# Performance work log

Hardware: AMD Instinct MI355X
Metric: run time of the kernel (lower is better)

Reference implementation:

```python
import jax, jax.numpy as jnp
import numpy as np

HEAD_SIZE = 64


def setup_inputs() -> dict:
    key = jax.random.key(0)
    ks = jax.random.split(key, 4)
    B, S, H, D = 8, 4096, 768, HEAD_SIZE
    scale = 1.0 / np.sqrt(H)
    return {
        "x": jax.random.normal(ks[0], (B, S, H), dtype=jnp.float32),
        "Wq": jax.random.normal(ks[1], (H, D), dtype=jnp.float32) * scale,
        "bq": jnp.zeros((D,), dtype=jnp.float32),
        "Wk": jax.random.normal(ks[2], (H, D), dtype=jnp.float32) * scale,
        "bk": jnp.zeros((D,), dtype=jnp.float32),
        "Wv": jax.random.normal(ks[3], (H, D), dtype=jnp.float32) * scale,
        "bv": jnp.zeros((D,), dtype=jnp.float32),
    }


def reference(x, Wq, bq, Wk, bk, Wv, bv):
    # x: [B, S, H]
    B, S, H = x.shape
    D = Wq.shape[1]
    q = x @ Wq + bq  # [B, S, D]
    k = x @ Wk + bk
    v = x @ Wv + bv
    # naive full score matrix [B, S, S]
    scores = jnp.einsum("bsd,btd->bst", q, k)
    causal = jnp.tril(jnp.ones((S, S), dtype=bool))  # lower-triangular mask
    scores = jnp.where(causal[None, :, :], scores, -jnp.inf)
    attn = jax.nn.softmax(scores / jnp.sqrt(jnp.float32(D)), axis=-1)
    # dropout is identity in eval/deterministic reference
    out = jnp.einsum("bst,btd->bsd", attn, v)  # [B, S, D]
    return out
```

## Files before the change

kernel.cpp:

```cpp
#include <hip/hip_runtime.h>

typedef unsigned short u16;
typedef __bf16 bf16_t;
typedef bf16_t bf16x8 __attribute__((ext_vector_type(8)));
typedef float f32x4 __attribute__((ext_vector_type(4)));
typedef u16 u16x8 __attribute__((ext_vector_type(8)));
typedef u16 u16x4 __attribute__((ext_vector_type(4)));
typedef unsigned u32x4 __attribute__((ext_vector_type(4)));

#define B_ 8
#define S_ 4096
#define H_ 768
#define M_ (B_ * S_)

__device__ __forceinline__ u16 f2b(float f) {
  unsigned u = __float_as_uint(f);
  u += 0x7fffu + ((u >> 16) & 1u);
  return (u16)(u >> 16);
}

__device__ __forceinline__ void gl_lds16(const void* g, void* l) {
  __builtin_amdgcn_global_load_lds(
      (const __attribute__((address_space(1))) void*)g,
      (__attribute__((address_space(3))) void*)l, 16, 0, 0);
}

__global__ __launch_bounds__(256) void wconv_k(const float* __restrict__ Wq,
                                               const float* __restrict__ Wk,
                                               const float* __restrict__ Wv,
                                               u16* __restrict__ WbT) {
  __shared__ float wt[64 * 68];
  const int tid = threadIdx.x;
  int mat = blockIdx.x / 12;
  int k0 = (blockIdx.x % 12) * 64;
  const float* W = (mat == 0) ? Wq : ((mat == 1) ? Wk : Wv);
  int r = tid >> 2, c0 = (tid & 3) * 16;
  const float* src = W + (size_t)(k0 + r) * 64 + c0;
#pragma unroll
  for (int j = 0; j < 16; j += 4)
    *(float4*)&wt[r * 68 + c0 + j] = *(const float4*)(src + j);
  __syncthreads();
  int d = tid >> 2;
  u16* dst = WbT + (size_t)(mat * 64 + d) * 768 + k0 + c0;
  u16x8 o0, o1;
#pragma unroll
  for (int j = 0; j < 8; ++j) o0[j] = f2b(wt[(c0 + j) * 68 + d]);
#pragma unroll
  for (int j = 0; j < 8; ++j) o1[j] = f2b(wt[(c0 + 8 + j) * 68 + d]);
  *(u16x8*)dst = o0;
  *(u16x8*)(dst + 8) = o1;
}

__global__ __launch_bounds__(256) void qkv_k(const float* __restrict__ x,
                                             const u16* __restrict__ WbT,
                                             const float* __restrict__ bq,
                                             const float* __restrict__ bk,
                                             const float* __restrict__ bv,
                                             u16* __restrict__ qb,
                                             u16* __restrict__ kb,
                                             u16* __restrict__ vbT) {
  __shared__ __align__(16) u16 smem[2 * 2560 + 2 * 7680];
  const int tid = threadIdx.x;
  const int w = tid >> 6, ln = tid & 15, qd = (tid >> 4) & 3;
  const int row0 = blockIdx.x * 64;

  const f32x4 z4 = {0.f, 0.f, 0.f, 0.f};
  f32x4 acc[4][3];
#pragma unroll
  for (int rt = 0; rt < 4; ++rt)
#pragma unroll
    for (int ct = 0; ct < 3; ++ct) acc[rt][ct] = z4;

  const int xr = tid >> 2, xc = (tid & 3) * 8;
  float4 xf0, xf1;
  u16x8 wf[3];

  auto load_t = [&](int kt) {
    const float* sx = x + (size_t)(row0 + xr) * 768 + kt * 32 + xc;
    xf0 = *(const float4*)sx;
    xf1 = *(const float4*)(sx + 4);
#pragma unroll
    for (int i = 0; i < 3; ++i) {
      int c = i * 256 + tid;
      int r = c >> 2, off = (c & 3) * 8;
      wf[i] = *(const u16x8*)(WbT + (size_t)r * 768 + kt * 32 + off);
    }
  };

  load_t(0);
  for (int kt = 0; kt < 24; ++kt) {
    u16* xs = smem + (kt & 1) * 2560;
    u16* wsb = smem + 5120 + (kt & 1) * 7680;
    {
      u16x8 v;
      v[0] = f2b(xf0.x); v[1] = f2b(xf0.y); v[2] = f2b(xf0.z); v[3] = f2b(xf0.w);
      v[4] = f2b(xf1.x); v[5] = f2b(xf1.y); v[6] = f2b(xf1.z); v[7] = f2b(xf1.w);
      *(u16x8*)&xs[xr * 40 + xc] = v;
#pragma unroll
      for (int i = 0; i < 3; ++i) {
        int c = i * 256 + tid;
        int r = c >> 2, off = (c & 3) * 8;
        *(u16x8*)&wsb[r * 40 + off] = wf[i];
      }
    }
    if (kt < 23) load_t(kt + 1);
    __syncthreads();
    bf16x8 af[4], bfr[3];
#pragma unroll
    for (int rt = 0; rt < 4; ++rt)
      af[rt] = *(const bf16x8*)&xs[(rt * 16 + ln) * 40 + qd * 8];
#pragma unroll
    for (int ct = 0; ct < 3; ++ct)
      bfr[ct] = *(const bf16x8*)&wsb[(w * 48 + ct * 16 + ln) * 40 + qd * 8];
#pragma unroll
    for (int rt = 0; rt < 4; ++rt)
#pragma unroll
      for (int ct = 0; ct < 3; ++ct)
        acc[rt][ct] = __builtin_amdgcn_mfma_f32_16x16x32_bf16(
            af[rt], bfr[ct], acc[rt][ct], 0, 0, 0);
    __syncthreads();
  }

  u16* vt = smem;
#pragma unroll
  for (int ct = 0; ct < 3; ++ct) {
    int col = w * 48 + ct * 16 + ln;
    int mat = col >> 6, d = col & 63;
    if (mat < 2) {
      const float* bp = (mat == 0) ? bq : bk;
      u16* op = (mat == 0) ? qb : kb;
      float bias = bp[d];
      float scale = (mat == 0) ? 0.18033688011112042f : 1.0f;
#pragma unroll
      for (int rt = 0; rt < 4; ++rt)
#pragma unroll
        for (int r = 0; r < 4; ++r)
          op[(size_t)(row0 + rt * 16 + qd * 4 + r) * 64 + d] =
              f2b((acc[rt][ct][r] + bias) * scale);
    } else {
      float bias = bv[d];
#pragma unroll
      for (int rt = 0; rt < 4; ++rt)
#pragma unroll
        for (int r = 0; r < 4; ++r)
          vt[d * 72 + rt * 16 + qd * 4 + r] = f2b(acc[rt][ct][r] + bias);
    }
  }
  __syncthreads();
  {
    int d = tid >> 2, so = (tid & 3) * 16;
    int b = row0 >> 12, s0 = row0 & 4095;
    u16* dst = vbT + ((size_t)b * 64 + d) * 4096 + s0;
#pragma unroll
    for (int g = 0; g < 4; ++g) {
      int ts = so + g * 4;
      int tn = (ts & 0x23) | ((ts & 4) << 2) | ((ts & 0x18) >> 1);
      *(u16x4*)(dst + ts) = *(const u16x4*)&vt[d * 72 + tn];
    }
  }
}

__global__ __launch_bounds__(256) void attn_k(const u16* __restrict__ qb,
                                              const u16* __restrict__ kb,
                                              const u16* __restrict__ vbT,
                                              float* __restrict__ po,
                                              float* __restrict__ pl) {
  __shared__ __align__(16) u16 ks[3][4096];
  __shared__ __align__(16) u16 vs[3][4096];
  const int tid = threadIdx.x;
  const int wv = tid >> 6, ln = tid & 15, qd = (tid >> 4) & 3;
  const int id = blockIdx.x;
  const int b = id & 7;
  const int j = id >> 3;
  int qi = 31, acc = 0;
  while (acc + ((qi >> 3) + 1) <= j) {
    acc += (qi >> 3) + 1;
    --qi;
  }
  const int c = j - acc;
  const int ntiles = 2 * qi + 2;
  const int nc = (qi >> 3) + 1;
  const int bas = ntiles / nc, rem = ntiles % nc;
  const int tstart = c * bas + (c < rem ? c : rem);
  const int tcount = bas + (c < rem ? 1 : 0);
  const int q0 = qi * 128;
  const int q0w = q0 + wv * 32;
  const int base = b * S_;
  const u16* kg = kb + (size_t)base * 64;
  const u16* vg = vbT + (size_t)b * 64 * 4096;

  bf16x8 qf[2][2];
#pragma unroll
  for (int qt = 0; qt < 2; ++qt) {
    const u16* qrow = qb + (size_t)(base + q0w + qt * 16 + ln) * 64;
    qf[qt][0] = *(const bf16x8*)(qrow + qd * 8);
    qf[qt][1] = *(const bf16x8*)(qrow + 32 + qd * 8);
  }
  const f32x4 z4 = {0.f, 0.f, 0.f, 0.f};
  f32x4 o0[4] = {z4, z4, z4, z4};
  f32x4 o1[4] = {z4, z4, z4, z4};
  float lq0 = 0.f, lq1 = 0.f;
  const int lr = (tid & 63) >> 3, csl = tid & 7;

  auto prefetch = [&](int bufi, int tile) {
    const u16* kt_ = kg + (size_t)tile * 4096;
    const u16* vt_ = vg + tile * 64;
#pragma unroll
    for (int i = 0; i < 2; ++i) {
      int r0 = wv * 16 + i * 8;
      int r = r0 + lr;
      int cc = csl ^ (r & 7);
      gl_lds16(kt_ + r * 64 + cc * 8, &ks[bufi][r0 * 64]);
      gl_lds16(vt_ + (size_t)r * 4096 + cc * 8, &vs[bufi][r0 * 64]);
    }
  };

  prefetch(0, tstart);
  prefetch(1, tstart + (tcount > 1 ? 1 : 0));
  int cur = 0, pfb = 2;
  for (int it = 0; it < tcount; ++it) {
    asm volatile("s_waitcnt vmcnt(4)" ::: "memory");
    __builtin_amdgcn_s_barrier();
    int nx = it + 2;
    nx = nx < tcount ? nx : tcount - 1;
    prefetch(pfb, tstart + nx);
    const int t0a = (tstart + it) * 64;

    if (t0a <= q0w + 31) {
      f32x4 s0[4] = {z4, z4, z4, z4};
      f32x4 s1[4] = {z4, z4, z4, z4};
      __builtin_amdgcn_s_setprio(1);
#pragma unroll
      for (int kc = 0; kc < 2; ++kc) {
        int cs = (kc * 4 + qd) ^ (ln & 7);
#pragma unroll
        for (int nt = 0; nt < 4; ++nt) {
          bf16x8 kf = *(const bf16x8*)&ks[cur][(nt * 16 + ln) * 64 + cs * 8];
          s0[nt] = __builtin_amdgcn_mfma_f32_16x16x32_bf16(kf, qf[0][kc], s0[nt], 0, 0, 0);
          s1[nt] = __builtin_amdgcn_mfma_f32_16x16x32_bf16(kf, qf[1][kc], s1[nt], 0, 0, 0);
        }
      }
      __builtin_amdgcn_s_setprio(0);
      if (t0a + 63 > q0w) {
#pragma unroll
        for (int nt = 0; nt < 4; ++nt) {
          int tg = t0a + nt * 16 + qd * 4;
#pragma unroll
          for (int r = 0; r < 4; ++r) {
            if (tg + r > q0w + ln) s0[nt][r] = -INFINITY;
            if (tg + r > q0w + 16 + ln) s1[nt][r] = -INFINITY;
          }
        }
      }
      float p0[4][4], p1[4][4];
#pragma unroll
      for (int nt = 0; nt < 4; ++nt)
#pragma unroll
        for (int r = 0; r < 4; ++r) {
          p0[nt][r] = __builtin_amdgcn_exp2f(s0[nt][r]);
          p1[nt][r] = __builtin_amdgcn_exp2f(s1[nt][r]);
          lq0 += p0[nt][r];
          lq1 += p1[nt][r];
        }
      unsigned pk0[8], pk1[8];
#pragma unroll
      for (int i = 0; i < 8; ++i) {
        int nt = i >> 1, rb = (i & 1) * 2;
        asm("v_cvt_pk_bf16_f32 %0, %1, %2"
            : "=v"(pk0[i]) : "v"(p0[nt][rb]), "v"(p0[nt][rb + 1]));
        asm("v_cvt_pk_bf16_f32 %0, %1, %2"
            : "=v"(pk1[i]) : "v"(p1[nt][rb]), "v"(p1[nt][rb + 1]));
      }
      __builtin_amdgcn_s_setprio(1);
#pragma unroll
      for (int kc = 0; kc < 2; ++kc) {
        u32x4 w0 = {pk0[4 * kc], pk0[4 * kc + 1], pk0[4 * kc + 2], pk0[4 * kc + 3]};
        u32x4 w1 = {pk1[4 * kc], pk1[4 * kc + 1], pk1[4 * kc + 2], pk1[4 * kc + 3]};
        bf16x8 a0 = __builtin_bit_cast(bf16x8, w0);
        bf16x8 a1 = __builtin_bit_cast(bf16x8, w1);
        int cs = (kc * 4 + qd) ^ (ln & 7);
#pragma unroll
        for (int nt = 0; nt < 4; ++nt) {
          bf16x8 vf = *(const bf16x8*)&vs[cur][(nt * 16 + ln) * 64 + cs * 8];
          o0[nt] = __builtin_amdgcn_mfma_f32_16x16x32_bf16(a0, vf, o0[nt], 0, 0, 0);
          o1[nt] = __builtin_amdgcn_mfma_f32_16x16x32_bf16(a1, vf, o1[nt], 0, 0, 0);
        }
      }
      __builtin_amdgcn_s_setprio(0);
    }
    cur = (cur == 2) ? 0 : cur + 1;
    pfb = (pfb == 2) ? 0 : pfb + 1;
  }

  lq0 += __shfl_xor(lq0, 16);
  lq0 += __shfl_xor(lq0, 32);
  lq1 += __shfl_xor(lq1, 16);
  lq1 += __shfl_xor(lq1, 32);

  float* op = po + (size_t)c * 2097152;
  float* lpt = pl + (size_t)c * 32768;
#pragma unroll
  for (int r = 0; r < 4; ++r) {
    int row0 = base + q0w + qd * 4 + r;
    int row1 = row0 + 16;
#pragma unroll
    for (int nt = 0; nt < 4; ++nt) {
      op[(size_t)row0 * 64 + nt * 16 + ln] = o0[nt][r];
      op[(size_t)row1 * 64 + nt * 16 + ln] = o1[nt][r];
    }
  }
  if (qd == 0) {
    lpt[base + q0w + ln] = lq0;
    lpt[base + q0w + 16 + ln] = lq1;
  }
}

__global__ __launch_bounds__(256) void comb_k(const float* __restrict__ po,
                                              const float* __restrict__ pl,
                                              float* __restrict__ out) {
  int idx = blockIdx.x * 256 + threadIdx.x;
  int r = idx >> 4, d0 = (idx & 15) * 4;
  int qi = (r & 4095) >> 7;
  int nc = (qi >> 3) + 1;
  const float* p = po + (size_t)r * 64 + d0;
  float4 a = *(const float4*)p;
  float l = pl[r];
  if (nc > 1) {
    float4 t = *(const float4*)(p + 2097152);
    a.x += t.x; a.y += t.y; a.z += t.z; a.w += t.w;
    l += pl[r + 32768];
  }
  if (nc > 2) {
    float4 t = *(const float4*)(p + 4194304);
    a.x += t.x; a.y += t.y; a.z += t.z; a.w += t.w;
    l += pl[r + 65536];
  }
  if (nc > 3) {
    float4 t = *(const float4*)(p + 6291456);
    a.x += t.x; a.y += t.y; a.z += t.z; a.w += t.w;
    l += pl[r + 98304];
  }
  float inv = 1.0f / l;
  a.x *= inv; a.y *= inv; a.z *= inv; a.w *= inv;
  *(float4*)(out + (size_t)r * 64 + d0) = a;
}

extern "C" void kernel_launch(void* const* d_in, const int* in_sizes, int n_in,
                              void* d_out, int out_size, void* d_ws, size_t ws_size,
                              hipStream_t stream) {
  const float* x  = (const float*)d_in[0];
  const float* Wq = (const float*)d_in[1];
  const float* bq = (const float*)d_in[2];
  const float* Wk = (const float*)d_in[3];
  const float* bk = (const float*)d_in[4];
  const float* Wv = (const float*)d_in[5];
  const float* bv = (const float*)d_in[6];
  float* out = (float*)d_out;

  char* wsp = (char*)d_ws;
  u16* WbT = (u16*)wsp;
  u16* qb  = (u16*)(wsp + 294912);
  u16* kb  = (u16*)(wsp + 4489216);
  u16* vbT = (u16*)(wsp + 8683520);
  float* po = (float*)(wsp + 12877824);
  float* pl = (float*)(wsp + 46432256);

  hipLaunchKernelGGL(wconv_k, dim3(36), dim3(256), 0, stream, Wq, Wk, Wv, WbT);
  hipLaunchKernelGGL(qkv_k, dim3(512), dim3(256), 0, stream,
                     x, WbT, bq, bk, bv, qb, kb, vbT);
  hipLaunchKernelGGL(attn_k, dim3(640), dim3(256), 0, stream,
                     qb, kb, vbT, po, pl);
  hipLaunchKernelGGL(comb_k, dim3(2048), dim3(256), 0, stream,
                     po, pl, out);
}
```

Before: 213.0 us.

## Double query tile per block to 256 rows and compute row sums via MFMA

Each attention block now handles 256 query rows (64 per wave, four 16-row subtiles) instead of 128, so every K/V tile loaded into LDS is reused across twice as many queries. The key-split schedule is rebalanced with a new chunk-count formula, giving a smaller grid, and the combine kernel loops over a variable number of partials. Softmax denominators are now accumulated with an extra MFMA against a ones vector, replacing scalar adds and shuffles. The cost is higher register pressure from four times more accumulators, which may lower occupancy, and coarser causal-masking granularity that wastes more work on diagonal tiles.

```diff
diff --git a/kernel.cpp b/kernel.cpp
--- a/kernel.cpp
+++ b/kernel.cpp
@@ -172,34 +172,44 @@
   const int id = blockIdx.x;
   const int b = id & 7;
   const int j = id >> 3;
-  int qi = 31, acc = 0;
-  while (acc + ((qi >> 3) + 1) <= j) {
-    acc += (qi >> 3) + 1;
-    --qi;
+  int qi = 15, acc = 0;
+  for (;;) {
+    int ncq = (4 * qi + 13) / 10;
+    if (acc + ncq <= j) { acc += ncq; --qi; } else break;
   }
   const int c = j - acc;
-  const int ntiles = 2 * qi + 2;
-  const int nc = (qi >> 3) + 1;
+  const int ntiles = 4 * qi + 4;
+  const int nc = (4 * qi + 13) / 10;
   const int bas = ntiles / nc, rem = ntiles % nc;
   const int tstart = c * bas + (c < rem ? c : rem);
   const int tcount = bas + (c < rem ? 1 : 0);
-  const int q0 = qi * 128;
-  const int q0w = q0 + wv * 32;
+  const int q0 = qi * 256;
+  const int q0w = q0 + wv * 64;
   const int base = b * S_;
   const u16* kg = kb + (size_t)base * 64;
   const u16* vg = vbT + (size_t)b * 64 * 4096;
 
-  bf16x8 qf[2][2];
-#pragma unroll
-  for (int qt = 0; qt < 2; ++qt) {
+  bf16x8 qf[4][2];
+#pragma unroll
+  for (int qt = 0; qt < 4; ++qt) {
     const u16* qrow = qb + (size_t)(base + q0w + qt * 16 + ln) * 64;
     qf[qt][0] = *(const bf16x8*)(qrow + qd * 8);
     qf[qt][1] = *(const bf16x8*)(qrow + 32 + qd * 8);
   }
   const f32x4 z4 = {0.f, 0.f, 0.f, 0.f};
-  f32x4 o0[4] = {z4, z4, z4, z4};
-  f32x4 o1[4] = {z4, z4, z4, z4};
-  float lq0 = 0.f, lq1 = 0.f;
+  f32x4 o[4][4];
+#pragma unroll
+  for (int qt = 0; qt < 4; ++qt)
+#pragma unroll
+    for (int nt = 0; nt < 4; ++nt) o[qt][nt] = z4;
+  f32x4 lacc[4] = {z4, z4, z4, z4};
+  bf16x8 bones;
+  {
+    u16x8 u;
+#pragma unroll
+    for (int i = 0; i < 8; ++i) u[i] = 0x3F80;
+    bones = __builtin_bit_cast(bf16x8, u);
+  }
   const int lr = (tid & 63) >> 3, csl = tid & 7;
 
   auto prefetch = [&](int bufi, int tile) {
@@ -226,9 +236,12 @@
     prefetch(pfb, tstart + nx);
     const int t0a = (tstart + it) * 64;
 
-    if (t0a <= q0w + 31) {
-      f32x4 s0[4] = {z4, z4, z4, z4};
-      f32x4 s1[4] = {z4, z4, z4, z4};
+    if (t0a <= q0w + 63) {
+      f32x4 s[4][4];
+#pragma unroll
+      for (int qt = 0; qt < 4; ++qt)
+#pragma unroll
+        for (int nt = 0; nt < 4; ++nt) s[qt][nt] = z4;
       __builtin_amdgcn_s_setprio(1);
 #pragma unroll
       for (int kc = 0; kc < 2; ++kc) {
@@ -236,55 +249,60 @@
 #pragma unroll
         for (int nt = 0; nt < 4; ++nt) {
           bf16x8 kf = *(const bf16x8*)&ks[cur][(nt * 16 + ln) * 64 + cs * 8];
-          s0[nt] = __builtin_amdgcn_mfma_f32_16x16x32_bf16(kf, qf[0][kc], s0[nt], 0, 0, 0);
-          s1[nt] = __builtin_amdgcn_mfma_f32_16x16x32_bf16(kf, qf[1][kc], s1[nt], 0, 0, 0);
+#pragma unroll
+          for (int qt = 0; qt < 4; ++qt)
+            s[qt][nt] = __builtin_amdgcn_mfma_f32_16x16x32_bf16(
+                kf, qf[qt][kc], s[qt][nt], 0, 0, 0);
         }
       }
       __builtin_amdgcn_s_setprio(0);
       if (t0a + 63 > q0w) {
 #pragma unroll
-        for (int nt = 0; nt < 4; ++nt) {
-          int tg = t0a + nt * 16 + qd * 4;
-#pragma unroll
-          for (int r = 0; r < 4; ++r) {
-            if (tg + r > q0w + ln) s0[nt][r] = -INFINITY;
-            if (tg + r > q0w + 16 + ln) s1[nt][r] = -INFINITY;
+        for (int qt = 0; qt < 4; ++qt) {
+          int qrow = q0w + qt * 16 + ln;
+#pragma unroll
+          for (int nt = 0; nt < 4; ++nt) {
+            int tg = t0a + nt * 16 + qd * 4;
+#pragma unroll
+            for (int r = 0; r < 4; ++r)
+              if (tg + r > qrow) s[qt][nt][r] = -INFINITY;
           }
         }
       }
-      float p0[4][4], p1[4][4];
-#pragma unroll
-      for (int nt = 0; nt < 4; ++nt)
-#pragma unroll
-        for (int r = 0; r < 4; ++r) {
-          p0[nt][r] = __builtin_amdgcn_exp2f(s0[nt][r]);
-          p1[nt][r] = __builtin_amdgcn_exp2f(s1[nt][r]);
-          lq0 += p0[nt][r];
-          lq1 += p1[nt][r];
-        }
-      unsigned pk0[8], pk1[8];
-#pragma unroll
-      for (int i = 0; i < 8; ++i) {
-        int nt = i >> 1, rb = (i & 1) * 2;
-        asm("v_cvt_pk_bf16_f32 %0, %1, %2"
-            : "=v"(pk0[i]) : "v"(p0[nt][rb]), "v"(p0[nt][rb + 1]));
-        asm("v_cvt_pk_bf16_f32 %0, %1, %2"
-            : "=v"(pk1[i]) : "v"(p1[nt][rb]), "v"(p1[nt][rb + 1]));
-      }
+      unsigned pk[4][8];
+#pragma unroll
+      for (int qt = 0; qt < 4; ++qt)
+#pragma unroll
+        for (int i = 0; i < 8; ++i) {
+          int nt = i >> 1, rb = (i & 1) * 2;
+          float pa = __builtin_amdgcn_exp2f(s[qt][nt][rb]);
+          float pb = __builtin_amdgcn_exp2f(s[qt][nt][rb + 1]);
+          asm("v_cvt_pk_bf16_f32 %0, %1, %2"
+              : "=v"(pk[qt][i]) : "v"(pa), "v"(pb));
+        }
       __builtin_amdgcn_s_setprio(1);
 #pragma unroll
       for (int kc = 0; kc < 2; ++kc) {
-        u32x4 w0 = {pk0[4 * kc], pk0[4 * kc + 1], pk0[4 * kc + 2], pk0[4 * kc + 3]};
-        u32x4 w1 = {pk1[4 * kc], pk1[4 * kc + 1], pk1[4 * kc + 2], pk1[4 * kc + 3]};
-        bf16x8 a0 = __builtin_bit_cast(bf16x8, w0);
-        bf16x8 a1 = __builtin_bit_cast(bf16x8, w1);
+        bf16x8 a[4];
+#pragma unroll
+        for (int qt = 0; qt < 4; ++qt) {
+          u32x4 wd = {pk[qt][4 * kc], pk[qt][4 * kc + 1],
+                      pk[qt][4 * kc + 2], pk[qt][4 * kc + 3]};
+          a[qt] = __builtin_bit_cast(bf16x8, wd);
+        }
         int cs = (kc * 4 + qd) ^ (ln & 7);
 #pragma unroll
         for (int nt = 0; nt < 4; ++nt) {
           bf16x8 vf = *(const bf16x8*)&vs[cur][(nt * 16 + ln) * 64 + cs * 8];
-          o0[nt] = __builtin_amdgcn_mfma_f32_16x16x32_bf16(a0, vf, o0[nt], 0, 0, 0);
-          o1[nt] = __builtin_amdgcn_mfma_f32_16x16x32_bf16(a1, vf, o1[nt], 0, 0, 0);
-        }
+#pragma unroll
+          for (int qt = 0; qt < 4; ++qt)
+            o[qt][nt] = __builtin_amdgcn_mfma_f32_16x16x32_bf16(
+                a[qt], vf, o[qt][nt], 0, 0, 0);
+        }
+#pragma unroll
+        for (int qt = 0; qt < 4; ++qt)
+          lacc[qt] = __builtin_amdgcn_mfma_f32_16x16x32_bf16(
+              a[qt], bones, lacc[qt], 0, 0, 0);
       }
       __builtin_amdgcn_s_setprio(0);
     }
@@ -292,26 +310,18 @@
     pfb = (pfb == 2) ? 0 : pfb + 1;
   }
 
-  lq0 += __shfl_xor(lq0, 16);
-  lq0 += __shfl_xor(lq0, 32);
-  lq1 += __shfl_xor(lq1, 16);
-  lq1 += __shfl_xor(lq1, 32);
-
   float* op = po + (size_t)c * 2097152;
   float* lpt = pl + (size_t)c * 32768;
 #pragma unroll
-  for (int r = 0; r < 4; ++r) {
-    int row0 = base + q0w + qd * 4 + r;
-    int row1 = row0 + 16;
-#pragma unroll
-    for (int nt = 0; nt < 4; ++nt) {
-      op[(size_t)row0 * 64 + nt * 16 + ln] = o0[nt][r];
-      op[(size_t)row1 * 64 + nt * 16 + ln] = o1[nt][r];
-    }
-  }
-  if (qd == 0) {
-    lpt[base + q0w + ln] = lq0;
-    lpt[base + q0w + 16 + ln] = lq1;
+  for (int qt = 0; qt < 4; ++qt) {
+#pragma unroll
+    for (int r = 0; r < 4; ++r) {
+      int row = base + q0w + qt * 16 + qd * 4 + r;
+#pragma unroll
+      for (int nt = 0; nt < 4; ++nt)
+        op[(size_t)row * 64 + nt * 16 + ln] = o[qt][nt][r];
+      if (ln == 0) lpt[row] = lacc[qt][r];
+    }
   }
 }
 
@@ -320,25 +330,15 @@
                                               float* __restrict__ out) {
   int idx = blockIdx.x * 256 + threadIdx.x;
   int r = idx >> 4, d0 = (idx & 15) * 4;
-  int qi = (r & 4095) >> 7;
-  int nc = (qi >> 3) + 1;
+  int qi = (r & 4095) >> 8;
+  int nc = (4 * qi + 13) / 10;
   const float* p = po + (size_t)r * 64 + d0;
   float4 a = *(const float4*)p;
   float l = pl[r];
-  if (nc > 1) {
-    float4 t = *(const float4*)(p + 2097152);
+  for (int cc = 1; cc < nc; ++cc) {
+    float4 t = *(const float4*)(p + (size_t)cc * 2097152);
     a.x += t.x; a.y += t.y; a.z += t.z; a.w += t.w;
-    l += pl[r + 32768];
-  }
-  if (nc > 2) {
-    float4 t = *(const float4*)(p + 4194304);
-    a.x += t.x; a.y += t.y; a.z += t.z; a.w += t.w;
-    l += pl[r + 65536];
-  }
-  if (nc > 3) {
-    float4 t = *(const float4*)(p + 6291456);
-    a.x += t.x; a.y += t.y; a.z += t.z; a.w += t.w;
-    l += pl[r + 98304];
+    l += pl[r + cc * 32768];
   }
   float inv = 1.0f / l;
   a.x *= inv; a.y *= inv; a.z *= inv; a.w *= inv;
@@ -363,12 +363,12 @@
   u16* kb  = (u16*)(wsp + 4489216);
   u16* vbT = (u16*)(wsp + 8683520);
   float* po = (float*)(wsp + 12877824);
-  float* pl = (float*)(wsp + 46432256);
+  float* pl = (float*)(wsp + 71598080);
 
   hipLaunchKernelGGL(wconv_k, dim3(36), dim3(256), 0, stream, Wq, Wk, Wv, WbT);
   hipLaunchKernelGGL(qkv_k, dim3(512), dim3(256), 0, stream,
                      x, WbT, bq, bk, bv, qb, kb, vbT);
-  hipLaunchKernelGGL(attn_k, dim3(640), dim3(256), 0, stream,
+  hipLaunchKernelGGL(attn_k, dim3(488), dim3(256), 0, stream,
                      qb, kb, vbT, po, pl);
   hipLaunchKernelGGL(comb_k, dim3(2048), dim3(256), 0, stream,
                      po, pl, out);
```

Result: slower. 224.2 us (+5.2%).

## Split causal KV range into more chunks and switch attention to double buffering

Applied to the files above, without the earlier changes.

The attention kernel now splits each query tile's causal key range into roughly twice as many chunks, growing the grid from 640 to 1152 blocks, to improve load balance and GPU fill. The LDS K/V staging drops from triple to double buffering with a full vmcnt wait, which lowers shared memory per block but exposes more load latency. The combine kernel sums up to 8 partials through a loop, and the partial buffer is enlarged to match. The QKV projection also drops the trailing per-iteration barrier in its k-loop, which could race between LDS reads and the next tile's writes.

```diff
diff --git a/kernel.cpp b/kernel.cpp
--- a/kernel.cpp
+++ b/kernel.cpp
@@ -118,8 +118,8 @@
       for (int ct = 0; ct < 3; ++ct)
         acc[rt][ct] = __builtin_amdgcn_mfma_f32_16x16x32_bf16(
             af[rt], bfr[ct], acc[rt][ct], 0, 0, 0);
-    __syncthreads();
-  }
+  }
+  __syncthreads();
 
   u16* vt = smem;
 #pragma unroll
@@ -165,21 +165,21 @@
                                               const u16* __restrict__ vbT,
                                               float* __restrict__ po,
                                               float* __restrict__ pl) {
-  __shared__ __align__(16) u16 ks[3][4096];
-  __shared__ __align__(16) u16 vs[3][4096];
+  __shared__ __align__(16) u16 ks[2][4096];
+  __shared__ __align__(16) u16 vs[2][4096];
   const int tid = threadIdx.x;
   const int wv = tid >> 6, ln = tid & 15, qd = (tid >> 4) & 3;
   const int id = blockIdx.x;
   const int b = id & 7;
   const int j = id >> 3;
   int qi = 31, acc = 0;
-  while (acc + ((qi >> 3) + 1) <= j) {
-    acc += (qi >> 3) + 1;
-    --qi;
+  for (;;) {
+    int ncq = (2 * qi + 9) >> 3;
+    if (acc + ncq <= j) { acc += ncq; --qi; } else break;
   }
   const int c = j - acc;
   const int ntiles = 2 * qi + 2;
-  const int nc = (qi >> 3) + 1;
+  const int nc = (2 * qi + 9) >> 3;
   const int bas = ntiles / nc, rem = ntiles % nc;
   const int tstart = c * bas + (c < rem ? c : rem);
   const int tcount = bas + (c < rem ? 1 : 0);
@@ -216,14 +216,11 @@
   };
 
   prefetch(0, tstart);
-  prefetch(1, tstart + (tcount > 1 ? 1 : 0));
-  int cur = 0, pfb = 2;
+  int cur = 0;
   for (int it = 0; it < tcount; ++it) {
-    asm volatile("s_waitcnt vmcnt(4)" ::: "memory");
+    asm volatile("s_waitcnt vmcnt(0)" ::: "memory");
     __builtin_amdgcn_s_barrier();
-    int nx = it + 2;
-    nx = nx < tcount ? nx : tcount - 1;
-    prefetch(pfb, tstart + nx);
+    if (it + 1 < tcount) prefetch(cur ^ 1, tstart + it + 1);
     const int t0a = (tstart + it) * 64;
 
     if (t0a <= q0w + 31) {
@@ -288,8 +285,7 @@
       }
       __builtin_amdgcn_s_setprio(0);
     }
-    cur = (cur == 2) ? 0 : cur + 1;
-    pfb = (pfb == 2) ? 0 : pfb + 1;
+    cur ^= 1;
   }
 
   lq0 += __shfl_xor(lq0, 16);
@@ -321,24 +317,14 @@
   int idx = blockIdx.x * 256 + threadIdx.x;
   int r = idx >> 4, d0 = (idx & 15) * 4;
   int qi = (r & 4095) >> 7;
-  int nc = (qi >> 3) + 1;
+  int nc = (2 * qi + 9) >> 3;
   const float* p = po + (size_t)r * 64 + d0;
   float4 a = *(const float4*)p;
   float l = pl[r];
-  if (nc > 1) {
-    float4 t = *(const float4*)(p + 2097152);
+  for (int cc = 1; cc < nc; ++cc) {
+    float4 t = *(const float4*)(p + (size_t)cc * 2097152);
     a.x += t.x; a.y += t.y; a.z += t.z; a.w += t.w;
-    l += pl[r + 32768];
-  }
-  if (nc > 2) {
-    float4 t = *(const float4*)(p + 4194304);
-    a.x += t.x; a.y += t.y; a.z += t.z; a.w += t.w;
-    l += pl[r + 65536];
-  }
-  if (nc > 3) {
-    float4 t = *(const float4*)(p + 6291456);
-    a.x += t.x; a.y += t.y; a.z += t.z; a.w += t.w;
-    l += pl[r + 98304];
+    l += pl[r + cc * 32768];
   }
   float inv = 1.0f / l;
   a.x *= inv; a.y *= inv; a.z *= inv; a.w *= inv;
@@ -363,12 +349,12 @@
   u16* kb  = (u16*)(wsp + 4489216);
   u16* vbT = (u16*)(wsp + 8683520);
   float* po = (float*)(wsp + 12877824);
-  float* pl = (float*)(wsp + 46432256);
+  float* pl = (float*)(wsp + 79986688);
 
   hipLaunchKernelGGL(wconv_k, dim3(36), dim3(256), 0, stream, Wq, Wk, Wv, WbT);
   hipLaunchKernelGGL(qkv_k, dim3(512), dim3(256), 0, stream,
                      x, WbT, bq, bk, bv, qb, kb, vbT);
-  hipLaunchKernelGGL(attn_k, dim3(640), dim3(256), 0, stream,
+  hipLaunchKernelGGL(attn_k, dim3(1152), dim3(256), 0, stream,
                      qb, kb, vbT, po, pl);
   hipLaunchKernelGGL(comb_k, dim3(2048), dim3(256), 0, stream,
                      po, pl, out);
```

After: 212.2 us. Within noise of the previous version (-0.4%).
